# Kernel tuning notes

Hardware: AMD Instinct MI355X
Metric: run time of the kernel (lower is better)

## Reference

```python
import jax, jax.numpy as jnp
import numpy as np

D = 128            # actual_dim
DM = 2 * D         # d_model = 256
DI = 2 * DM        # support-encoder inner dim = 512
H = 2 * DM         # LSTMCell hidden = 512
NUM_SYMBOLS = 200000
KNN_K = 10
PROCESS_STEPS = 4
BQ, BS, NN = 4096, 128, 64


def setup_inputs() -> dict:
    key = jax.random.key(0)
    ks = jax.random.split(key, 20)
    ri = lambda k, shape, hi: jax.random.randint(k, shape, 0, hi)
    rn = lambda k, shape, s=0.05: jax.random.normal(k, shape, jnp.float32) * s
    emb = rn(ks[0], (NUM_SYMBOLS + 1, D), 0.1).at[NUM_SYMBOLS].set(0.0)  # padding row
    return {
        "query": ri(ks[1], (BQ, 2), NUM_SYMBOLS),
        "support": ri(ks[2], (BS, 2), NUM_SYMBOLS),
        "q_l_conn": ri(ks[3], (BQ, NN, 2), NUM_SYMBOLS),
        "q_l_deg": ri(ks[4], (BQ,), NN),
        "q_r_conn": ri(ks[5], (BQ, NN, 2), NUM_SYMBOLS),
        "q_r_deg": ri(ks[6], (BQ,), NN),
        "s_l_conn": ri(ks[7], (BS, NN, 2), NUM_SYMBOLS),
        "s_l_deg": ri(ks[8], (BS,), NN),
        "s_r_conn": ri(ks[9], (BS, NN, 2), NUM_SYMBOLS),
        "s_r_deg": ri(ks[10], (BS,), NN),
        "emb": emb,
        "gcn_W": rn(ks[11], (D, 2 * D)),
        "gcn_wb": jnp.zeros((D,), jnp.float32),
        "gcn_b": jnp.zeros((D,), jnp.float32),
        "se_w1": rn(ks[12], (DI, DM)),
        "se_b1": jnp.zeros((DI,), jnp.float32),
        "se_w2": rn(ks[13], (DM, DI)),
        "se_b2": jnp.zeros((DM,), jnp.float32),
        "ln_g": jnp.ones((DM,), jnp.float32),
        "ln_b": jnp.zeros((DM,), jnp.float32),
        "W_ih": rn(ks[14], (4 * H, DM)),
        "W_hh": rn(ks[15], (4 * H, H)),
        "b_ih": jnp.zeros((4 * H,), jnp.float32),
        "b_hh": jnp.zeros((4 * H,), jnp.float32),
    }


def _cos(a, b, eps=1e-8):
    num = jnp.sum(a * b, -1)
    den = jnp.maximum(jnp.linalg.norm(a, axis=-1), eps) * jnp.maximum(jnp.linalg.norm(b, axis=-1), eps)
    return num / den


def _neighbor_encoder(emb, gcn_W, gcn_wb, gcn_b, conn, ent_ids):
    rel = emb[conn[..., 0]]                     # [B,N,D]
    ent = emb[conn[..., 1]]                     # [B,N,D]
    center = emb[ent_ids][:, None, :]           # [B,1,D]
    sim = _cos(center, ent)                     # [B,N]
    _, idx = jax.lax.top_k(sim, KNN_K)          # [B,K]
    rel_k = jnp.take_along_axis(rel, idx[..., None], axis=1)
    ent_k = jnp.take_along_axis(ent, idx[..., None], axis=1)
    cat = jnp.concatenate([rel_k, ent_k], -1)   # [B,K,2D]
    h = jnp.einsum('bkf,df->bkd', cat, gcn_W) + gcn_wb + gcn_b
    return jnp.tanh(h.mean(axis=1))             # [B,D]


def _support_encoder(x, w1, b1, w2, b2, g, b):
    # residual FFN + LayerNorm (GMatching SupportEncoder), dropout off (eval)
    out = jax.nn.relu(x @ w1.T + b1) @ w2.T + b2
    y = out + x
    mu = y.mean(-1, keepdims=True)
    var = ((y - mu) ** 2).mean(-1, keepdims=True)
    return (y - mu) / jnp.sqrt(var + 1e-5) * g + b


def _query_encoder(support, query, W_ih, W_hh, b_ih, b_hh):
    # GMatching attentive LSTM process block. support: [1,DM], query: [B,DM]
    B = query.shape[0]
    h_r = jnp.zeros((B, H), query.dtype)
    c = jnp.zeros((B, H), query.dtype)
    h = query
    for _ in range(PROCESS_STEPS):
        gates = query @ W_ih.T + b_ih + h_r @ W_hh.T + b_hh
        i, f, g_, o = jnp.split(gates, 4, axis=-1)  # torch LSTMCell gate order
        c = jax.nn.sigmoid(f) * c + jax.nn.sigmoid(i) * jnp.tanh(g_)
        h_new = jax.nn.sigmoid(o) * jnp.tanh(c)     # [B,H]
        h = query + h_new[:, :DM]                   # [B,DM]
        attn = jax.nn.softmax(h @ support.T, axis=1)  # [B,1]
        r = attn @ support                          # [B,DM]
        h_r = jnp.concatenate([h, r], axis=1)       # [B,H]
    return h


def reference(query, support, q_l_conn, q_l_deg, q_r_conn, q_r_deg,
              s_l_conn, s_l_deg, s_r_conn, s_r_deg,
              emb, gcn_W, gcn_wb, gcn_b,
              se_w1, se_b1, se_w2, se_b2, ln_g, ln_b,
              W_ih, W_hh, b_ih, b_hh):
    ne = lambda conn, ids: _neighbor_encoder(emb, gcn_W, gcn_wb, gcn_b, conn, ids)
    q_nb = jnp.concatenate([ne(q_l_conn, query[:, 0]), ne(q_r_conn, query[:, 1])], -1)    # [BQ,DM]
    s_nb = jnp.concatenate([ne(s_l_conn, support[:, 0]), ne(s_r_conn, support[:, 1])], -1)  # [BS,DM]
    se = lambda x: _support_encoder(x, se_w1, se_b1, se_w2, se_b2, ln_g, ln_b)
    support_g = se(s_nb).mean(axis=0, keepdims=True)  # [1,DM]
    query_g = se(q_nb)                                # [BQ,DM]
    qf = _query_encoder(support_g, query_g, W_ih, W_hh, b_ih, b_hh)
    l2 = lambda x: x / jnp.maximum(jnp.linalg.norm(x, axis=-1, keepdims=True), 1e-12)
    return (l2(qf) @ l2(support_g).T).squeeze(-1)     # [BQ]
```

## Files before the change

### kernel.cpp

```cpp
#include <hip/hip_runtime.h>
#include <hip/hip_bf16.h>

#define D   128
#define DM  256
#define DI  512
#define HH  512
#define KNN 10
#define NN  64
#define BQ  4096
#define BS  128
#define BM2 (BQ + BS)
#define G2  1024
#define GK  256
#define NSYM 200000

__device__ __forceinline__ float sigmoidf_(float x) {
    return 1.f / (1.f + __expf(-x));
}
__device__ __forceinline__ float tanh_fast(float x) {
    x = fminf(fmaxf(x, -20.f), 20.f);
    float e = __expf(2.f * x);
    return (e - 1.f) / (e + 1.f);
}
__device__ __forceinline__ ushort f2bf(float x) {
    union { float f; unsigned u; } v; v.f = x;
    unsigned r = (v.u + 0x7fffu + ((v.u >> 16) & 1u)) >> 16;
    return (ushort)r;
}

typedef __bf16  bf16x8  __attribute__((ext_vector_type(8)));
typedef float   floatx4 __attribute__((ext_vector_type(4)));

__global__ __launch_bounds__(256) void prep_kernel(
    const float* __restrict__ emb, float* __restrict__ norms,
    const float* __restrict__ W_ih, const float* __restrict__ W_hh,
    const float* __restrict__ b_ih, const float* __restrict__ b_hh,
    const float* __restrict__ se_w1, const float* __restrict__ se_w2,
    ushort* __restrict__ wih_bf, ushort* __restrict__ whh_bf,
    float* __restrict__ bsumP, ushort* __restrict__ w1_bf,
    ushort* __restrict__ w2_bf)
{
    int bid = blockIdx.x;
    int tid = threadIdx.x;
    if (bid < 50000) {
        int wave = tid >> 6, lane = tid & 63;
        int row = bid * 4 + wave;
        float2 v = *(const float2*)&emb[(size_t)row * D + lane * 2];
        float s = v.x * v.x + v.y * v.y;
        #pragma unroll
        for (int off = 32; off; off >>= 1) s += __shfl_xor(s, off);
        if (lane == 0) norms[row] = sqrtf(s);
    } else if (bid < 50000 + G2) {
        int n = bid - 50000;
        int bn = n >> 7, r = n & 127;
        int half = (r >> 6) & 1, j = (r >> 4) & 3, l = r & 15;
        int u = bn * 32 + half * 16 + l;
        int oldrow = j * 512 + u;
        wih_bf[n * 256 + tid] = f2bf(W_ih[(size_t)oldrow * DM + tid]);
        whh_bf[n * 256 + tid] = f2bf(W_hh[(size_t)oldrow * HH + tid]);
        if (tid == 0) bsumP[n] = b_ih[oldrow] + b_hh[oldrow];
    } else {
        int idx = (bid - 50000 - G2) * 256 + tid;
        w1_bf[idx] = f2bf(se_w1[idx]);
        w2_bf[idx] = f2bf(se_w2[idx]);
    }
}

__global__ __launch_bounds__(256) void ne_kernel(
    const int* __restrict__ q_l, const int* __restrict__ q_r,
    const int* __restrict__ q_ids,
    const int* __restrict__ s_l, const int* __restrict__ s_r,
    const int* __restrict__ s_ids,
    const float* __restrict__ emb, const float* __restrict__ norms,
    float* __restrict__ catm_out)
{
    int bid = blockIdx.x;
    const int *conn_l, *conn_r, *ids;
    int row;
    if (bid < BQ * 2) { conn_l = q_l; conn_r = q_r; ids = q_ids; row = bid >> 1; }
    else { conn_l = s_l; conn_r = s_r; ids = s_ids; row = (bid - BQ * 2) >> 1; }
    int side = bid & 1;
    const int* conn = (side ? conn_r : conn_l) + (size_t)row * NN * 2;
    int cid = ids[row * 2 + side];

    __shared__ int   connb[NN * 2];
    __shared__ float sim[NN];
    __shared__ int   selr[KNN], sele[KNN];

    int tid = threadIdx.x;
    int wave = tid >> 6, lane = tid & 63;
    int grp = lane >> 4, l16 = lane & 15;

    if (tid < NN * 2) connb[tid] = conn[tid];
    const float* cp = &emb[(size_t)cid * D + l16 * 8];
    float4 c4a = *(const float4*)cp;
    float4 c4b = *(const float4*)(cp + 4);
    float cnorm = fmaxf(norms[cid], 1e-8f);
    __syncthreads();

    float4 ea[4], eb[4];
    #pragma unroll
    for (int b = 0; b < 4; b++) {
        int j = wave * 16 + b * 4 + grp;
        int eid = connb[j * 2 + 1];
        const float* ep = &emb[(size_t)eid * D + l16 * 8];
        ea[b] = *(const float4*)ep;
        eb[b] = *(const float4*)(ep + 4);
    }
    #pragma unroll
    for (int b = 0; b < 4; b++) {
        int j = wave * 16 + b * 4 + grp;
        float dot = c4a.x * ea[b].x + c4a.y * ea[b].y + c4a.z * ea[b].z + c4a.w * ea[b].w
                  + c4b.x * eb[b].x + c4b.y * eb[b].y + c4b.z * eb[b].z + c4b.w * eb[b].w;
        #pragma unroll
        for (int off = 8; off; off >>= 1) dot += __shfl_xor(dot, off);
        if (l16 == 0) sim[j] = dot / cnorm;
    }
    __syncthreads();
    if (tid < NN) sim[tid] = sim[tid] / fmaxf(norms[connb[tid * 2 + 1]], 1e-8f);
    __syncthreads();

    if (wave == 0) {
        float s = sim[lane];
        int id = lane;
        for (int k = 0; k < KNN; k++) {
            float bs = s; int bi = id;
            #pragma unroll
            for (int off = 32; off; off >>= 1) {
                float os = __shfl_xor(bs, off);
                int   oi = __shfl_xor(bi, off);
                if (os > bs || (os == bs && oi < bi)) { bs = os; bi = oi; }
            }
            if (lane == 0) { selr[k] = connb[bi * 2]; sele[k] = connb[bi * 2 + 1]; }
            if (id == bi) s = -__builtin_inff();
        }
    }
    __syncthreads();

    float acc = 0.f;
    if (tid < D) {
        #pragma unroll
        for (int k = 0; k < KNN; k++) acc += emb[(size_t)selr[k] * D + tid];
    } else {
        int d = tid - D;
        #pragma unroll
        for (int k = 0; k < KNN; k++) acc += emb[(size_t)sele[k] * D + d];
    }
    catm_out[(size_t)bid * DM + tid] = acc * (1.f / KNN);
}

#define GR 16
__global__ __launch_bounds__(256) void gcn_kernel(
    const float* __restrict__ catm, const float* __restrict__ gcn_W,
    const float* __restrict__ gcn_wb, const float* __restrict__ gcn_b,
    float* __restrict__ out, ushort* __restrict__ out_bf)
{
    __shared__ float cs[GR][DM];
    __shared__ float pp[GR][DM];
    int tid = threadIdx.x;
    int m0 = blockIdx.x * GR;
    #pragma unroll
    for (int t = 0; t < 4; t++) {
        int chunk = tid + 256 * t;
        int r = chunk >> 6, c4 = chunk & 63;
        *(float4*)&cs[r][c4 * 4] = *(const float4*)&catm[(size_t)(m0 + r) * DM + c4 * 4];
    }
    __syncthreads();

    int d = tid & 127, half = tid >> 7;
    float a[GR];
    #pragma unroll
    for (int r = 0; r < GR; r++) a[r] = 0.f;
    const float4* W4 = (const float4*)(gcn_W + (size_t)d * DM + half * D);
    for (int f4 = 0; f4 < D / 4; ++f4) {
        float4 w = W4[f4];
        #pragma unroll
        for (int r = 0; r < GR; r++) {
            const float* c = &cs[r][half * D + f4 * 4];
            a[r] += w.x * c[0] + w.y * c[1] + w.z * c[2] + w.w * c[3];
        }
    }
    #pragma unroll
    for (int r = 0; r < GR; r++) pp[r][tid] = a[r];
    __syncthreads();
    if (tid < D) {
        #pragma unroll
        for (int r = 0; r < GR; r++) {
            float h = pp[r][tid] + pp[r][tid + D] + gcn_wb[tid] + gcn_b[tid];
            float th = tanh_fast(h);
            out[(size_t)(m0 + r) * D + tid] = th;
            out_bf[(size_t)(m0 + r) * D + tid] = f2bf(th);
        }
    }
}

#define BMT 128
#define BNT 128
#define BKT 64
#define LDP (BKT + 8)

#define GEMM_CORE(AP, BP, KDIM)                                               \
    floatx4 acc[4][4];                                                        \
    _Pragma("unroll")                                                         \
    for (int i = 0; i < 4; i++)                                               \
        _Pragma("unroll")                                                     \
        for (int j = 0; j < 4; j++) acc[i][j] = (floatx4){0.f, 0.f, 0.f, 0.f};\
    for (int k0 = 0; k0 < (KDIM); k0 += BKT) {                                \
        __syncthreads();                                                      \
        _Pragma("unroll")                                                     \
        for (int t = 0; t < 4; t++) {                                         \
            int chunk = tid + 256 * t;                                        \
            int r = chunk >> 3;                                               \
            int c8 = (chunk & 7) * 8;                                         \
            *(uint4*)&As[r][c8] = *(const uint4*)&(AP)[(size_t)(bm * BMT + r) * (KDIM) + k0 + c8]; \
            *(uint4*)&Bs[r][c8] = *(const uint4*)&(BP)[(size_t)(bn * BNT + r) * (KDIM) + k0 + c8]; \
        }                                                                     \
        __syncthreads();                                                      \
        _Pragma("unroll")                                                     \
        for (int kk = 0; kk < BKT; kk += 32) {                                \
            bf16x8 af[4], bf[4];                                              \
            _Pragma("unroll")                                                 \
            for (int i = 0; i < 4; i++)                                       \
                af[i] = *(const bf16x8*)&As[wm + i * 16 + l16][kk + quad * 8];\
            _Pragma("unroll")                                                 \
            for (int j = 0; j < 4; j++)                                       \
                bf[j] = *(const bf16x8*)&Bs[wn + j * 16 + l16][kk + quad * 8];\
            _Pragma("unroll")                                                 \
            for (int i = 0; i < 4; i++)                                       \
                _Pragma("unroll")                                             \
                for (int j = 0; j < 4; j++)                                   \
                    acc[i][j] = __builtin_amdgcn_mfma_f32_16x16x32_bf16(      \
                        af[i], bf[j], acc[i][j], 0, 0, 0);                    \
        }                                                                     \
    }

#define GEMM_PRE()                                                            \
    __shared__ __align__(16) ushort As[BMT][LDP];                             \
    __shared__ __align__(16) ushort Bs[BNT][LDP];                             \
    int tid = threadIdx.x;                                                    \
    int wave = tid >> 6, lane = tid & 63;                                     \
    int quad = lane >> 4, l16 = lane & 15;                                    \
    int bm = blockIdx.x, bn = blockIdx.y;                                     \
    int wm = (wave >> 1) * 64, wn = (wave & 1) * 64;                          \
    (void)wave;

__global__ __launch_bounds__(256) void se_gemm1_kernel(
    const ushort* __restrict__ A, const ushort* __restrict__ B,
    const float* __restrict__ b1, ushort* __restrict__ Cbf)
{
    GEMM_PRE();
    GEMM_CORE(A, B, DM);
    #pragma unroll
    for (int i = 0; i < 4; i++) {
        #pragma unroll
        for (int j = 0; j < 4; j++) {
            int row = bm * BMT + wm + i * 16 + quad * 4;
            int col = bn * BNT + wn + j * 16 + l16;
            float bb = b1[col];
            #pragma unroll
            for (int rr = 0; rr < 4; rr++)
                Cbf[(size_t)(row + rr) * DI + col] = f2bf(fmaxf(acc[i][j][rr] + bb, 0.f));
        }
    }
}

__global__ __launch_bounds__(256) void se_gemm2_kernel(
    const ushort* __restrict__ A, const ushort* __restrict__ B,
    const float* __restrict__ b2, const float* __restrict__ xres,
    float* __restrict__ C)
{
    GEMM_PRE();
    GEMM_CORE(A, B, DI);
    #pragma unroll
    for (int i = 0; i < 4; i++) {
        #pragma unroll
        for (int j = 0; j < 4; j++) {
            int row = bm * BMT + wm + i * 16 + quad * 4;
            int col = bn * BNT + wn + j * 16 + l16;
            float bb = b2[col];
            #pragma unroll
            for (int rr = 0; rr < 4; rr++)
                C[(size_t)(row + rr) * DM + col] =
                    acc[i][j][rr] + bb + xres[(size_t)(row + rr) * DM + col];
        }
    }
}

#define LN_ROWS 8
__global__ __launch_bounds__(256) void ln_kernel(
    const float* __restrict__ ys, const float* __restrict__ g,
    const float* __restrict__ b, float* __restrict__ outf,
    ushort* __restrict__ outbf)
{
    int tid = threadIdx.x;
    int wave = tid >> 6, lane = tid & 63;
    int r0 = blockIdx.x * LN_ROWS;
    for (int rr = 0; rr < 2; ++rr) {
        int r = r0 + wave * 2 + rr;
        float vals[4];
        float s = 0.f;
        #pragma unroll
        for (int e = 0; e < 4; e++) {
            vals[e] = ys[(size_t)r * DM + e * 64 + lane];
            s += vals[e];
        }
        #pragma unroll
        for (int off = 32; off; off >>= 1) s += __shfl_xor(s, off);
        float mu = s * (1.f / DM);
        float v = 0.f;
        #pragma unroll
        for (int e = 0; e < 4; e++) { float dd = vals[e] - mu; v += dd * dd; }
        #pragma unroll
        for (int off = 32; off; off >>= 1) v += __shfl_xor(v, off);
        float rstd = rsqrtf(v * (1.f / DM) + 1e-5f);
        #pragma unroll
        for (int e = 0; e < 4; e++) {
            int dd = e * 64 + lane;
            float ov = (vals[e] - mu) * rstd * g[dd] + b[dd];
            outf[(size_t)r * DM + dd] = ov;
            outbf[(size_t)r * DM + dd] = f2bf(ov);
        }
    }
}

__global__ __launch_bounds__(256) void sgw_kernel(
    const float* __restrict__ ln_f, const float* __restrict__ W_hh,
    const float* __restrict__ b_ih, const float* __restrict__ b_hh,
    float* __restrict__ sg, float* __restrict__ gaddP)
{
    __shared__ float s[DM];
    int tid = threadIdx.x;
    float a = 0.f;
    for (int r = 0; r < BS; r++) a += ln_f[(size_t)(BQ + r) * DM + tid];
    a *= (1.f / BS);
    s[tid] = a;
    if (blockIdx.x == 0) sg[tid] = a;
    __syncthreads();

    int idx = blockIdx.x * 256 + tid;
    int g = idx >> 8, u = idx & 255;
    int oldrow = g * 512 + u;
    const float4* w4 = (const float4*)(W_hh + (size_t)oldrow * HH + DM);
    float acc = 0.f;
    for (int f4 = 0; f4 < DM / 4; ++f4) {
        float4 w = w4[f4];
        acc += w.x * s[f4 * 4] + w.y * s[f4 * 4 + 1] + w.z * s[f4 * 4 + 2] + w.w * s[f4 * 4 + 3];
    }
    float bs = b_ih[oldrow] + b_hh[oldrow];
    int n = (u >> 5) * 128 + ((u >> 4) & 1) * 64 + g * 16 + (u & 15);
    gaddP[n] = bs + acc;
}

__global__ __launch_bounds__(256) void lstm_gemm0_kernel(
    const ushort* __restrict__ A, const ushort* __restrict__ B,
    const float* __restrict__ bsumP, const float* __restrict__ lnf,
    float* __restrict__ P0f, float* __restrict__ Cf, ushort* __restrict__ h_out)
{
    GEMM_PRE();
    GEMM_CORE(A, B, GK);
    int u = bn * 32 + (wn ? 16 : 0) + l16;
    size_t tile = (size_t)bm * 8 + bn;
    float b4[4];
    #pragma unroll
    for (int j = 0; j < 4; j++) b4[j] = bsumP[bn * 128 + wn + j * 16 + l16];
    #pragma unroll
    for (int i = 0; i < 4; i++) {
        int row = bm * BMT + wm + i * 16 + quad * 4;
        #pragma unroll
        for (int j = 0; j < 4; j++)
            *(floatx4*)&P0f[((tile * 16 + i * 4 + j) * 256 + tid) * 4] = acc[i][j];
        floatx4 cv4;
        #pragma unroll
        for (int rr = 0; rr < 4; rr++) {
            float iv = acc[i][0][rr] + b4[0];
            float gv = acc[i][2][rr] + b4[2];
            float ov = acc[i][3][rr] + b4[3];
            float cv = sigmoidf_(iv) * tanh_fast(gv);
            cv4[rr] = cv;
            float h = lnf[(size_t)(row + rr) * DM + u] + sigmoidf_(ov) * tanh_fast(cv);
            h_out[(size_t)(row + rr) * DM + u] = f2bf(h);
        }
        *(floatx4*)&Cf[((tile * 4 + i) * 256 + tid) * 4] = cv4;
    }
}

__global__ __launch_bounds__(256) void lstm_step_kernel(
    const ushort* __restrict__ A, const ushort* __restrict__ B,
    const float* __restrict__ P0f, const float* __restrict__ gaddP,
    const float* __restrict__ lnf, float* __restrict__ Cf,
    ushort* __restrict__ h_out, float* __restrict__ hf_out, int last)
{
    GEMM_PRE();
    GEMM_CORE(A, B, GK);
    int u = bn * 32 + (wn ? 16 : 0) + l16;
    size_t tile = (size_t)bm * 8 + bn;
    float g4[4];
    #pragma unroll
    for (int j = 0; j < 4; j++) g4[j] = gaddP[bn * 128 + wn + j * 16 + l16];
    #pragma unroll
    for (int i = 0; i < 4; i++) {
        int row = bm * BMT + wm + i * 16 + quad * 4;
        floatx4 p0[4];
        #pragma unroll
        for (int j = 0; j < 4; j++)
            p0[j] = *(const floatx4*)&P0f[((tile * 16 + i * 4 + j) * 256 + tid) * 4];
        floatx4 cprev = *(const floatx4*)&Cf[((tile * 4 + i) * 256 + tid) * 4];
        floatx4 cnew;
        #pragma unroll
        for (int rr = 0; rr < 4; rr++) {
            float iv = acc[i][0][rr] + p0[0][rr] + g4[0];
            float fv = acc[i][1][rr] + p0[1][rr] + g4[1];
            float gv = acc[i][2][rr] + p0[2][rr] + g4[2];
            float ov = acc[i][3][rr] + p0[3][rr] + g4[3];
            float cv = sigmoidf_(fv) * cprev[rr] + sigmoidf_(iv) * tanh_fast(gv);
            cnew[rr] = cv;
            float h = lnf[(size_t)(row + rr) * DM + u] + sigmoidf_(ov) * tanh_fast(cv);
            if (last) hf_out[(size_t)(row + rr) * DM + u] = h;
            else      h_out[(size_t)(row + rr) * DM + u] = f2bf(h);
        }
        *(floatx4*)&Cf[((tile * 4 + i) * 256 + tid) * 4] = cnew;
    }
}

__global__ __launch_bounds__(256) void final_kernel(
    const float* __restrict__ h_ws, const float* __restrict__ sg,
    float* __restrict__ outp)
{
    __shared__ float sgs[DM];
    int tid = threadIdx.x;
    sgs[tid] = sg[tid];
    __syncthreads();
    int wave = tid >> 6, lane = tid & 63;
    float sn = 0.f;
    #pragma unroll
    for (int e = 0; e < 4; e++) { float v = sgs[e * 64 + lane]; sn += v * v; }
    #pragma unroll
    for (int off = 32; off; off >>= 1) sn += __shfl_xor(sn, off);
    float sgnorm = fmaxf(sqrtf(sn), 1e-12f);

    int row = blockIdx.x * 4 + wave;
    const float* h = h_ws + (size_t)row * DM;
    float dot = 0.f, hn = 0.f;
    #pragma unroll
    for (int e = 0; e < 4; e++) {
        float hv = h[e * 64 + lane];
        dot += hv * sgs[e * 64 + lane];
        hn += hv * hv;
    }
    #pragma unroll
    for (int off = 32; off; off >>= 1) { dot += __shfl_xor(dot, off); hn += __shfl_xor(hn, off); }
    if (lane == 0) outp[row] = dot / (fmaxf(sqrtf(hn), 1e-12f) * sgnorm);
}

extern "C" void kernel_launch(void* const* d_in, const int* in_sizes, int n_in,
                              void* d_out, int out_size, void* d_ws, size_t ws_size,
                              hipStream_t stream)
{
    const int* query    = (const int*)d_in[0];
    const int* support  = (const int*)d_in[1];
    const int* q_l_conn = (const int*)d_in[2];
    const int* q_r_conn = (const int*)d_in[4];
    const int* s_l_conn = (const int*)d_in[6];
    const int* s_r_conn = (const int*)d_in[8];
    const float* emb    = (const float*)d_in[10];
    const float* gcn_W  = (const float*)d_in[11];
    const float* gcn_wb = (const float*)d_in[12];
    const float* gcn_b  = (const float*)d_in[13];
    const float* se_w1  = (const float*)d_in[14];
    const float* se_b1  = (const float*)d_in[15];
    const float* se_w2  = (const float*)d_in[16];
    const float* se_b2  = (const float*)d_in[17];
    const float* ln_g   = (const float*)d_in[18];
    const float* ln_b   = (const float*)d_in[19];
    const float* W_ih   = (const float*)d_in[20];
    const float* W_hh   = (const float*)d_in[21];
    const float* b_ih   = (const float*)d_in[22];
    const float* b_hh   = (const float*)d_in[23];
    float* out = (float*)d_out;

    char* wsb = (char*)d_ws;
    float*  xf     = (float*)wsb;  wsb += (size_t)BM2 * DM * 4;
    ushort* xb     = (ushort*)wsb; wsb += (size_t)BM2 * DM * 2;
    ushort* t1_bf  = (ushort*)wsb; wsb += (size_t)BM2 * DI * 2;
    float*  ys     = (float*)wsb;  wsb += (size_t)BM2 * DM * 4;
    float*  ln_f   = (float*)wsb;  wsb += (size_t)BM2 * DM * 4;
    ushort* ln_bf  = (ushort*)wsb; wsb += (size_t)BM2 * DM * 2;
    float*  sg     = (float*)wsb;  wsb += DM * 4;
    float*  bsumP  = (float*)wsb;  wsb += G2 * 4;
    float*  gaddP  = (float*)wsb;  wsb += G2 * 4;
    ushort* wih_bf = (ushort*)wsb; wsb += (size_t)G2 * DM * 2;
    ushort* whh_bf = (ushort*)wsb; wsb += (size_t)G2 * DM * 2;
    ushort* w1_bf  = (ushort*)wsb; wsb += (size_t)DI * DM * 2;
    ushort* w2_bf  = (ushort*)wsb; wsb += (size_t)DM * DI * 2;
    float*  norms  = (float*)wsb;  wsb += (size_t)NSYM * 4;
    float*  P0f    = (float*)wsb;  wsb += (size_t)BQ * G2 * 4;
    float*  Cf     = (float*)wsb;  wsb += (size_t)BQ * DM * 4;
    ushort* h_bfA  = (ushort*)wsb; wsb += (size_t)BQ * DM * 2;
    ushort* h_bfB  = (ushort*)wsb; wsb += (size_t)BQ * DM * 2;
    float*  h_f    = (float*)wsb;  wsb += (size_t)BQ * DM * 4;

    float* catm = P0f;

    prep_kernel<<<50000 + G2 + 512, 256, 0, stream>>>(
        emb, norms, W_ih, W_hh, b_ih, b_hh, se_w1, se_w2,
        wih_bf, whh_bf, bsumP, w1_bf, w2_bf);
    ne_kernel<<<BQ * 2 + BS * 2, 256, 0, stream>>>(
        q_l_conn, q_r_conn, query, s_l_conn, s_r_conn, support,
        emb, norms, catm);
    gcn_kernel<<<(BM2 * 2) / GR, 256, 0, stream>>>(catm, gcn_W, gcn_wb, gcn_b,
                                                   xf, xb);
    { dim3 g1(BM2 / BMT, DI / BNT);
      se_gemm1_kernel<<<g1, 256, 0, stream>>>(xb, w1_bf, se_b1, t1_bf); }
    { dim3 g2(BM2 / BMT, DM / BNT);
      se_gemm2_kernel<<<g2, 256, 0, stream>>>(t1_bf, w2_bf, se_b2, xf, ys); }
    ln_kernel<<<BM2 / LN_ROWS, 256, 0, stream>>>(ys, ln_g, ln_b, ln_f, ln_bf);
    sgw_kernel<<<G2 / 256, 256, 0, stream>>>(ln_f, W_hh, b_ih, b_hh, sg, gaddP);

    dim3 ggrid(BQ / BMT, G2 / BNT);
    lstm_gemm0_kernel<<<ggrid, 256, 0, stream>>>(ln_bf, wih_bf, bsumP, ln_f,
                                                 P0f, Cf, h_bfA);
    lstm_step_kernel<<<ggrid, 256, 0, stream>>>(h_bfA, whh_bf, P0f, gaddP, ln_f,
                                                Cf, h_bfB, h_f, 0);
    lstm_step_kernel<<<ggrid, 256, 0, stream>>>(h_bfB, whh_bf, P0f, gaddP, ln_f,
                                                Cf, h_bfA, h_f, 0);
    lstm_step_kernel<<<ggrid, 256, 0, stream>>>(h_bfA, whh_bf, P0f, gaddP, ln_f,
                                                Cf, h_bfB, h_f, 1);
    final_kernel<<<BQ / 4, 256, 0, stream>>>(h_f, sg, out);
}
```

Before: 410.2 us.

## Use fp16 normalized embeddings for KNN scoring with fp32 refinement near cutoff

The prep kernel now also writes an fp16 copy of each embedding row, pre-normalized to unit length. The neighbor encoder scores cosine similarity from this half-size copy, finds the 11th-best score, and recomputes exact fp32 similarities only for candidates within a small margin of that threshold. It then rebuilds the mean vectors from the fp16 normalized rows multiplied back by their norms. This halves the bytes of the random gather in the hot kernel, at the cost of writing an extra fp16 table and a small precision loss in the aggregated embeddings.

```diff
diff --git a/kernel.cpp b/kernel.cpp
--- a/kernel.cpp
+++ b/kernel.cpp
@@ -1,5 +1,6 @@
 #include <hip/hip_runtime.h>
 #include <hip/hip_bf16.h>
+#include <hip/hip_fp16.h>
 
 #define D   128
 #define DM  256
@@ -13,6 +14,7 @@
 #define G2  1024
 #define GK  256
 #define NSYM 200000
+#define MARG 4e-3f
 
 __device__ __forceinline__ float sigmoidf_(float x) {
     return 1.f / (1.f + __expf(-x));
@@ -28,11 +30,14 @@
     return (ushort)r;
 }
 
-typedef __bf16  bf16x8  __attribute__((ext_vector_type(8)));
-typedef float   floatx4 __attribute__((ext_vector_type(4)));
+typedef __bf16    bf16x8  __attribute__((ext_vector_type(8)));
+typedef float     floatx4 __attribute__((ext_vector_type(4)));
+typedef _Float16  f16x8   __attribute__((ext_vector_type(8)));
+typedef _Float16  f16x2   __attribute__((ext_vector_type(2)));
 
 __global__ __launch_bounds__(256) void prep_kernel(
     const float* __restrict__ emb, float* __restrict__ norms,
+    _Float16* __restrict__ embn,
     const float* __restrict__ W_ih, const float* __restrict__ W_hh,
     const float* __restrict__ b_ih, const float* __restrict__ b_hh,
     const float* __restrict__ se_w1, const float* __restrict__ se_w2,
@@ -49,7 +54,13 @@
         float s = v.x * v.x + v.y * v.y;
         #pragma unroll
         for (int off = 32; off; off >>= 1) s += __shfl_xor(s, off);
-        if (lane == 0) norms[row] = sqrtf(s);
+        float nrm = sqrtf(s);
+        if (lane == 0) norms[row] = nrm;
+        float rinv = 1.f / fmaxf(nrm, 1e-8f);
+        f16x2 hv;
+        hv.x = (_Float16)(v.x * rinv);
+        hv.y = (_Float16)(v.y * rinv);
+        *(f16x2*)&embn[(size_t)row * D + lane * 2] = hv;
     } else if (bid < 50000 + G2) {
         int n = bid - 50000;
         int bn = n >> 7, r = n & 127;
@@ -71,7 +82,8 @@
     const int* __restrict__ q_ids,
     const int* __restrict__ s_l, const int* __restrict__ s_r,
     const int* __restrict__ s_ids,
-    const float* __restrict__ emb, const float* __restrict__ norms,
+    const float* __restrict__ emb, const _Float16* __restrict__ embn,
+    const float* __restrict__ norms,
     float* __restrict__ catm_out)
 {
     int bid = blockIdx.x;
@@ -85,45 +97,50 @@
 
     __shared__ int   connb[NN * 2];
     __shared__ float sim[NN];
-    __shared__ int   selr[KNN], sele[KNN];
+    __shared__ float sx[NN];
+    __shared__ int   candIdx[NN];
+    __shared__ int   ncand_sh;
+    __shared__ int   selr[KNN], sele[KNN], selj[KNN];
+    __shared__ _Float16 ents[NN][D];
 
     int tid = threadIdx.x;
     int wave = tid >> 6, lane = tid & 63;
     int grp = lane >> 4, l16 = lane & 15;
 
     if (tid < NN * 2) connb[tid] = conn[tid];
-    const float* cp = &emb[(size_t)cid * D + l16 * 8];
-    float4 c4a = *(const float4*)cp;
-    float4 c4b = *(const float4*)(cp + 4);
-    float cnorm = fmaxf(norms[cid], 1e-8f);
-    __syncthreads();
-
-    float4 ea[4], eb[4];
+    if (tid < NN) sx[tid] = -3.4e38f;
+    f16x8 c8 = *(const f16x8*)&embn[(size_t)cid * D + l16 * 8];
+    float cf[8];
+    #pragma unroll
+    for (int i = 0; i < 8; i++) cf[i] = (float)c8[i];
+    __syncthreads();
+
+    f16x8 ev[4];
     #pragma unroll
     for (int b = 0; b < 4; b++) {
         int j = wave * 16 + b * 4 + grp;
         int eid = connb[j * 2 + 1];
-        const float* ep = &emb[(size_t)eid * D + l16 * 8];
-        ea[b] = *(const float4*)ep;
-        eb[b] = *(const float4*)(ep + 4);
+        ev[b] = *(const f16x8*)&embn[(size_t)eid * D + l16 * 8];
     }
     #pragma unroll
     for (int b = 0; b < 4; b++) {
         int j = wave * 16 + b * 4 + grp;
-        float dot = c4a.x * ea[b].x + c4a.y * ea[b].y + c4a.z * ea[b].z + c4a.w * ea[b].w
-                  + c4b.x * eb[b].x + c4b.y * eb[b].y + c4b.z * eb[b].z + c4b.w * eb[b].w;
+        *(f16x8*)&ents[j][l16 * 8] = ev[b];
+        float dot = 0.f;
+        #pragma unroll
+        for (int i = 0; i < 8; i++) dot += cf[i] * (float)ev[b][i];
         #pragma unroll
         for (int off = 8; off; off >>= 1) dot += __shfl_xor(dot, off);
-        if (l16 == 0) sim[j] = dot / cnorm;
-    }
-    __syncthreads();
-    if (tid < NN) sim[tid] = sim[tid] / fmaxf(norms[connb[tid * 2 + 1]], 1e-8f);
-    __syncthreads();
-
+        if (l16 == 0) sim[j] = dot;
+    }
+    __syncthreads();
+
+    float s0 = 0.f, t11 = 0.f;
+    bool safe = false;
     if (wave == 0) {
-        float s = sim[lane];
-        int id = lane;
-        for (int k = 0; k < KNN; k++) {
+        s0 = sim[lane];
+        float s = s0; int id = lane;
+        for (int k = 0; k < KNN + 1; k++) {
             float bs = s; int bi = id;
             #pragma unroll
             for (int off = 32; off; off >>= 1) {
@@ -131,8 +148,58 @@
                 int   oi = __shfl_xor(bi, off);
                 if (os > bs || (os == bs && oi < bi)) { bs = os; bi = oi; }
             }
-            if (lane == 0) { selr[k] = connb[bi * 2]; sele[k] = connb[bi * 2 + 1]; }
+            t11 = bs;
             if (id == bi) s = -__builtin_inff();
+        }
+        safe = (s0 >= t11 + MARG);
+        bool cand = !safe && (s0 >= t11 - MARG);
+        unsigned long long cb = __ballot(cand);
+        if (cand) {
+            int pos = (int)__popcll(cb & ((1ull << lane) - 1ull));
+            candIdx[pos] = lane;
+        }
+        if (lane == 0) ncand_sh = (int)__popcll(cb);
+    }
+    __syncthreads();
+
+    {
+        int ncand = ncand_sh;
+        const float* cp = &emb[(size_t)cid * D + l16 * 8];
+        float4 C4a = *(const float4*)cp;
+        float4 C4b = *(const float4*)(cp + 4);
+        float cnorm = fmaxf(norms[cid], 1e-8f);
+        int team = wave * 4 + grp;
+        for (int c = team; c < ncand; c += 16) {
+            int j = candIdx[c];
+            int eid = connb[j * 2 + 1];
+            const float* ep = &emb[(size_t)eid * D + l16 * 8];
+            float4 a = *(const float4*)ep;
+            float4 b = *(const float4*)(ep + 4);
+            float dot = C4a.x * a.x + C4a.y * a.y + C4a.z * a.z + C4a.w * a.w
+                      + C4b.x * b.x + C4b.y * b.y + C4b.z * b.z + C4b.w * b.w;
+            #pragma unroll
+            for (int off = 8; off; off >>= 1) dot += __shfl_xor(dot, off);
+            if (l16 == 0) {
+                float t = dot / cnorm;
+                sx[j] = t / fmaxf(norms[eid], 1e-8f);
+            }
+        }
+    }
+    __syncthreads();
+
+    if (wave == 0) {
+        float key = safe ? 3.0e38f : sx[lane];
+        int id = lane;
+        for (int k = 0; k < KNN; k++) {
+            float bs = key; int bi = id;
+            #pragma unroll
+            for (int off = 32; off; off >>= 1) {
+                float os = __shfl_xor(bs, off);
+                int   oi = __shfl_xor(bi, off);
+                if (os > bs || (os == bs && oi < bi)) { bs = os; bi = oi; }
+            }
+            if (lane == 0) { selr[k] = connb[bi * 2]; sele[k] = connb[bi * 2 + 1]; selj[k] = bi; }
+            if (id == bi) key = -3.4e38f;
         }
     }
     __syncthreads();
@@ -140,11 +207,16 @@
     float acc = 0.f;
     if (tid < D) {
         #pragma unroll
-        for (int k = 0; k < KNN; k++) acc += emb[(size_t)selr[k] * D + tid];
+        for (int k = 0; k < KNN; k++) {
+            int r = selr[k];
+            acc += (float)embn[(size_t)r * D + tid] * norms[r];
+        }
     } else {
         int d = tid - D;
         #pragma unroll
-        for (int k = 0; k < KNN; k++) acc += emb[(size_t)sele[k] * D + d];
+        for (int k = 0; k < KNN; k++) {
+            acc += (float)ents[selj[k]][d] * norms[sele[k]];
+        }
     }
     catm_out[(size_t)bid * DM + tid] = acc * (1.f / KNN);
 }
@@ -479,12 +551,6 @@
     float* out = (float*)d_out;
 
     char* wsb = (char*)d_ws;
-    float*  xf     = (float*)wsb;  wsb += (size_t)BM2 * DM * 4;
-    ushort* xb     = (ushort*)wsb; wsb += (size_t)BM2 * DM * 2;
-    ushort* t1_bf  = (ushort*)wsb; wsb += (size_t)BM2 * DI * 2;
-    float*  ys     = (float*)wsb;  wsb += (size_t)BM2 * DM * 4;
-    float*  ln_f   = (float*)wsb;  wsb += (size_t)BM2 * DM * 4;
-    ushort* ln_bf  = (ushort*)wsb; wsb += (size_t)BM2 * DM * 2;
     float*  sg     = (float*)wsb;  wsb += DM * 4;
     float*  bsumP  = (float*)wsb;  wsb += G2 * 4;
     float*  gaddP  = (float*)wsb;  wsb += G2 * 4;
@@ -493,20 +559,30 @@
     ushort* w1_bf  = (ushort*)wsb; wsb += (size_t)DI * DM * 2;
     ushort* w2_bf  = (ushort*)wsb; wsb += (size_t)DM * DI * 2;
     float*  norms  = (float*)wsb;  wsb += (size_t)NSYM * 4;
-    float*  P0f    = (float*)wsb;  wsb += (size_t)BQ * G2 * 4;
-    float*  Cf     = (float*)wsb;  wsb += (size_t)BQ * DM * 4;
-    ushort* h_bfA  = (ushort*)wsb; wsb += (size_t)BQ * DM * 2;
-    ushort* h_bfB  = (ushort*)wsb; wsb += (size_t)BQ * DM * 2;
-    float*  h_f    = (float*)wsb;  wsb += (size_t)BQ * DM * 4;
-
-    float* catm = P0f;
+    float*  catm   = (float*)wsb;  wsb += (size_t)(BM2 * 2) * DM * 4;
+
+    char* ovl = wsb;
+    _Float16* embn = (_Float16*)ovl;
+
+    char* p = ovl;
+    float*  xf     = (float*)p;  p += (size_t)BM2 * DM * 4;
+    ushort* xb     = (ushort*)p; p += (size_t)BM2 * DM * 2;
+    ushort* t1_bf  = (ushort*)p; p += (size_t)BM2 * DI * 2;
+    float*  ys     = (float*)p;  p += (size_t)BM2 * DM * 4;
+    float*  ln_f   = (float*)p;  p += (size_t)BM2 * DM * 4;
+    ushort* ln_bf  = (ushort*)p; p += (size_t)BM2 * DM * 2;
+    float*  P0f    = (float*)p;  p += (size_t)BQ * G2 * 4;
+    float*  Cf     = (float*)p;  p += (size_t)BQ * DM * 4;
+    ushort* h_bfA  = (ushort*)p; p += (size_t)BQ * DM * 2;
+    ushort* h_bfB  = (ushort*)p; p += (size_t)BQ * DM * 2;
+    float*  h_f    = (float*)p;  p += (size_t)BQ * DM * 4;
 
     prep_kernel<<<50000 + G2 + 512, 256, 0, stream>>>(
-        emb, norms, W_ih, W_hh, b_ih, b_hh, se_w1, se_w2,
+        emb, norms, embn, W_ih, W_hh, b_ih, b_hh, se_w1, se_w2,
         wih_bf, whh_bf, bsumP, w1_bf, w2_bf);
     ne_kernel<<<BQ * 2 + BS * 2, 256, 0, stream>>>(
         q_l_conn, q_r_conn, query, s_l_conn, s_r_conn, support,
-        emb, norms, catm);
+        emb, embn, norms, catm);
     gcn_kernel<<<(BM2 * 2) / GR, 256, 0, stream>>>(catm, gcn_W, gcn_wb, gcn_b,
                                                    xf, xb);
     { dim3 g1(BM2 / BMT, DI / BNT);
```

Result: slower. 437.2 us (+6.6%).
